# Performance work log

Hardware: AMD Instinct MI355X
Metric: run time of the kernel (lower is better)

Reference implementation:

```python
import jax, jax.numpy as jnp
import numpy as np

N, E, D_IN, HID, OUT, H = 20000, 320000, 128, 128, 128, 4

def _lin(key, fan_in, fan_out):
    kw, kb = jax.random.split(key)
    W = jax.random.normal(kw, (fan_in, fan_out), jnp.float32) * 0.05
    b = jax.random.normal(kb, (fan_out,), jnp.float32) * 0.05
    return W, b

def setup_inputs() -> dict:
    key = jax.random.key(0)
    ks = jax.random.split(key, 10)
    x = jax.random.normal(ks[0], (N, D_IN), jnp.float32)
    edge_index = jax.random.randint(ks[1], (2, E), 0, N, jnp.int32)
    # Layer 0: TransformerConv(D_IN -> HID, heads=H, concat=True)
    Wq0, bq0 = _lin(ks[2], D_IN, H * HID)
    Wk0, bk0 = _lin(ks[3], D_IN, H * HID)
    Wv0, bv0 = _lin(ks[4], D_IN, H * HID)
    Ws0, bs0 = _lin(ks[5], D_IN, H * HID)   # root/skip projection
    # Layer 1: TransformerConv(H*HID -> OUT, heads=H, concat=False)
    Wq1, bq1 = _lin(ks[6], H * HID, H * OUT)
    Wk1, bk1 = _lin(ks[7], H * HID, H * OUT)
    Wv1, bv1 = _lin(ks[8], H * HID, H * OUT)
    Ws1, bs1 = _lin(ks[9], H * HID, OUT)    # skip maps to OUT when concat=False
    return dict(x=x, edge_index=edge_index,
                Wq0=Wq0, bq0=bq0, Wk0=Wk0, bk0=bk0, Wv0=Wv0, bv0=bv0, Ws0=Ws0, bs0=bs0,
                Wq1=Wq1, bq1=bq1, Wk1=Wk1, bk1=bk1, Wv1=Wv1, bv1=bv1, Ws1=Ws1, bs1=bs1)

def _transformer_conv(x, src, dst, Wq, bq, Wk, bk, Wv, bv, Ws, bs, heads, out_ch, concat):
    n = x.shape[0]
    q = (x @ Wq + bq).reshape(n, heads, out_ch)
    k = (x @ Wk + bk).reshape(n, heads, out_ch)
    v = (x @ Wv + bv).reshape(n, heads, out_ch)
    # per-edge attention logits: [E, H]
    alpha = jnp.einsum('ehc,ehc->eh', q[dst], k[src]) / jnp.sqrt(jnp.float32(out_ch))
    # softmax grouped by destination node (numerically stable)
    m = jax.ops.segment_max(alpha, dst, num_segments=n)        # [N, H]
    alpha = jnp.exp(alpha - m[dst])
    s = jax.ops.segment_sum(alpha, dst, num_segments=n)       # [N, H]
    alpha = alpha / (s[dst] + 1e-16)
    # weighted scatter-add of messages: [N, H, C]
    out = jax.ops.segment_sum(alpha[..., None] * v[src], dst, num_segments=n)
    if concat:
        out = out.reshape(n, heads * out_ch)
    else:
        out = out.mean(axis=1)
    return out + x @ Ws + bs  # root weight (skip connection)

def reference(x, edge_index,
              Wq0, bq0, Wk0, bk0, Wv0, bv0, Ws0, bs0,
              Wq1, bq1, Wk1, bk1, Wv1, bv1, Ws1, bs1):
    src, dst = edge_index[0], edge_index[1]
    h = _transformer_conv(x, src, dst, Wq0, bq0, Wk0, bk0, Wv0, bv0, Ws0, bs0, H, HID, True)
    h = jax.nn.relu(h)  # dropout is identity in eval mode
    out = _transformer_conv(h, src, dst, Wq1, bq1, Wk1, bk1, Wv1, bv1, Ws1, bs1, H, OUT, False)
    return out
```

## Files before the change

### kernel.cpp

```cpp
#include <hip/hip_runtime.h>
#include <hip/hip_bf16.h>
#include <math.h>

#define HCH    512
#define OUTD   128
#define N0CAT  2048
#define N1CAT  1664
#define P0STR  1024
#define P1STR  640
#define KVW    1024
#define DCAP   64

typedef __attribute__((ext_vector_type(8))) short short8v;
typedef __attribute__((ext_vector_type(8))) unsigned short ushort8v;
typedef __attribute__((ext_vector_type(4))) unsigned short ushort4v;
typedef __attribute__((ext_vector_type(4))) float floatx4;
typedef __attribute__((ext_vector_type(2))) float floatx2;
typedef __attribute__((ext_vector_type(4))) unsigned int uintx4;

__device__ inline float bf2f(unsigned short u) {
    return __uint_as_float(((unsigned)u) << 16);
}

__device__ inline unsigned short f2bf(float f) {
    return (unsigned short)__bfloat16_as_ushort(__float2bfloat16(f));
}

template <bool HI>
__device__ inline floatx2 fp8x2_to_f32(unsigned int w) {
    return __builtin_amdgcn_cvt_pk_f32_fp8(w, HI);
}

__device__ inline unsigned int f32x4_to_fp8(float a, float b, float c, float d) {
    int w = __builtin_amdgcn_cvt_pk_fp8_f32(a, b, 0, false);
    w = __builtin_amdgcn_cvt_pk_fp8_f32(c, d, w, true);
    return (unsigned int)w;
}

__device__ inline void gload_lds16(const void* g, void* l) {
    __builtin_amdgcn_global_load_lds(
        (const __attribute__((address_space(1))) unsigned int*)g,
        (__attribute__((address_space(3))) unsigned int*)l, 16, 0, 0);
}


__device__ void tpose_tile(const float* __restrict__ W, __hip_bfloat16* __restrict__ o,
                           int K, int C, int bx, int by, int t, float (*tile)[33],
                           int pmode) {
    int c0 = bx * 32, k0 = by * 32;
    int tx = t & 31, ty = t >> 5;
    #pragma unroll
    for (int r = ty; r < 32; r += 8)
        tile[r][tx] = W[(size_t)(k0 + r) * C + c0 + tx];
    __syncthreads();
    #pragma unroll
    for (int r = ty; r < 32; r += 8) {
        int col = c0 + r;
        if (pmode) col = ((col >> 3) << 4) + (col & 7) + ((pmode == 2) ? 8 : 0);
        o[(size_t)col * K + k0 + tx] = __float2bfloat16(tile[tx][r]);
    }
}

__global__ __launch_bounds__(256) void prep_all(
        const float* __restrict__ x, __hip_bfloat16* __restrict__ Xb,
        const float* __restrict__ Wq0, const float* __restrict__ Wk0,
        const float* __restrict__ Wv0, const float* __restrict__ Ws0,
        const float* __restrict__ Wq1, const float* __restrict__ Wk1,
        const float* __restrict__ Wv1, const float* __restrict__ Ws1,
        const float* __restrict__ bq0, const float* __restrict__ bk0,
        const float* __restrict__ bv0, const float* __restrict__ bs0,
        const float* __restrict__ bq1, const float* __restrict__ bk1,
        const float* __restrict__ bv1, const float* __restrict__ bs1,
        __hip_bfloat16* __restrict__ Wc0, __hip_bfloat16* __restrict__ Wc1,
        float* __restrict__ bc0, float* __restrict__ bc1,
        int* __restrict__ deg, int* __restrict__ srcs,
        const int* __restrict__ srce, const int* __restrict__ dste,
        int N, int E) {
    __shared__ float tile[32][33];
    int t = threadIdx.x;
    int b = blockIdx.x;
    int nb_cast = (N * 128 + 255) >> 8;
    if (b < nb_cast) {
        int i = b * 256 + t;
        if (i < N * 128) Xb[i] = __float2bfloat16(x[i]);
        return;
    }
    b -= nb_cast;
    if (b < 256) {
        int z = b >> 6, rem = b & 63;
        const float* W = (z == 0) ? Wq0 : (z == 1) ? Wk0 : (z == 2) ? Wv0 : Ws0;
        int base = (z == 0) ? 0 : (z == 3) ? 1536 : 512;
        int pmode = (z == 1) ? 1 : (z == 2) ? 2 : 0;
        tpose_tile(W, Wc0 + (size_t)base * 128, 128, 512, rem & 15, rem >> 4, t, tile, pmode);
        return;
    }
    b -= 256;
    if (b < 768) {
        int z = b >> 8, rem = b & 255;
        const float* W = (z == 0) ? Wq1 : (z == 1) ? Wk1 : Wv1;
        int base = (z == 0) ? 0 : 512;
        int pmode = (z == 1) ? 1 : (z == 2) ? 2 : 0;
        tpose_tile(W, Wc1 + (size_t)base * 512, 512, 512, rem & 15, rem >> 4, t, tile, pmode);
        return;
    }
    b -= 768;
    if (b < 64) {
        tpose_tile(Ws1, Wc1 + (size_t)1536 * 512, 512, 128, b & 3, b >> 2, t, tile, 0);
        return;
    }
    b -= 64;
    if (b < 8) {
        int i = b * 256 + t;
        if (i < N0CAT) {
            int sel = i >> 9, col = i & 511;
            const float* bb = (sel == 0) ? bq0 : (sel == 1) ? bk0 : (sel == 2) ? bv0 : bs0;
            int d = (sel == 0) ? i
                  : (sel == 3) ? i
                  : 512 + ((col >> 3) << 4) + (col & 7) + ((sel == 2) ? 8 : 0);
            bc0[d] = bb[col];
        }
        if (i < N1CAT) {
            if (i < 1536) {
                int sel = i >> 9, col = i & 511;
                const float* bb = (sel == 0) ? bq1 : (sel == 1) ? bk1 : bv1;
                int d = (sel == 0) ? i
                      : 512 + ((col >> 3) << 4) + (col & 7) + ((sel == 2) ? 8 : 0);
                bc1[d] = bb[col];
            } else {
                bc1[i] = bs1[i - 1536];
            }
        }
        return;
    }
    b -= 8;
    {
        int e = b * 256 + t;
        if (e < E) {
            int d = dste[e];
            int pos = atomicAdd(&deg[d], 1);
            if (pos < DCAP) srcs[d * DCAP + pos] = srce[e];
        }
    }
}


__device__ inline void gemm_store(floatx4 a, const float* __restrict__ bias,
                                  __hip_bfloat16* __restrict__ P, int pstride,
                                  unsigned char* __restrict__ KV8,
                                  int row, int col) {
    floatx4 bv = *(const floatx4*)(bias + col);
    float v0 = a[0] + bv[0];
    float v1 = a[1] + bv[1];
    float v2 = a[2] + bv[2];
    float v3 = a[3] + bv[3];
    if (col < 512) {
        ushort4v o = { f2bf(v0), f2bf(v1), f2bf(v2), f2bf(v3) };
        *(ushort4v*)(P + (size_t)row * pstride + col) = o;
    } else if (col < 1536) {
        *(unsigned int*)(KV8 + (size_t)row * KVW + (col - 512)) = f32x4_to_fp8(v0, v1, v2, v3);
    } else {
        ushort4v o = { f2bf(v0), f2bf(v1), f2bf(v2), f2bf(v3) };
        *(ushort4v*)(P + (size_t)row * pstride + 512 + (col - 1536)) = o;
    }
}


#define BM 128
#define BN 128
#define BK 64

__global__ __launch_bounds__(256) void gemm_mfma(const __hip_bfloat16* __restrict__ A,
                                                 const __hip_bfloat16* __restrict__ Bt,
                                                 const float* __restrict__ bias,
                                                 __hip_bfloat16* __restrict__ P,
                                                 int pstride,
                                                 unsigned char* __restrict__ KV8,
                                                 int M, int K, int Nd, int mt_pad) {
    __shared__ __hip_bfloat16 As[BM][BK];
    __shared__ __hip_bfloat16 Bs[BN][BK];
    int f = blockIdx.x;
    int mt = f % mt_pad, nt = f / mt_pad;
    int bm = mt * BM, bn = nt * BN;
    if (bm >= M) return;
    int t = threadIdx.x;
    int lane = t & 63, w = t >> 6;
    int quad = lane >> 4, l16 = lane & 15;
    int wm = (w >> 1) * 64, wn = (w & 1) * 64;

    int srow = w * 8 + (lane >> 3);
    int c8g = (lane & 7) ^ ((lane >> 3) & 7);
    const char* Ab = (const char*)(A + (size_t)(bm + srow) * K + c8g * 8);
    const char* Bb = (const char*)(Bt + (size_t)(bn + srow) * K + c8g * 8);
    char* Al = (char*)&As[0][0] + w * 1024;
    char* Bl = (char*)&Bs[0][0] + w * 1024;

    int sw = l16 & 7;

    floatx4 acc[4][4];
    #pragma unroll
    for (int i = 0; i < 4; i++)
        #pragma unroll
        for (int j = 0; j < 4; j++)
            acc[i][j] = (floatx4)0.0f;

    for (int k0 = 0; k0 < K; k0 += BK) {
        __syncthreads();
        #pragma unroll
        for (int i = 0; i < 4; i++) {
            size_t go = ((size_t)i * 32 * K + k0) * 2;
            gload_lds16(Ab + go, Al + i * 4096);
            gload_lds16(Bb + go, Bl + i * 4096);
        }
        __syncthreads();
        #pragma unroll
        for (int ks = 0; ks < BK; ks += 32) {
            int c8a = (quad + (ks >> 3)) ^ sw;
            short8v af[4], bfr[4];
            #pragma unroll
            for (int i = 0; i < 4; i++)
                af[i] = *(const short8v*)&As[wm + i * 16 + l16][c8a * 8];
            #pragma unroll
            for (int j = 0; j < 4; j++)
                bfr[j] = *(const short8v*)&Bs[wn + j * 16 + l16][c8a * 8];
            #pragma unroll
            for (int i = 0; i < 4; i++)
                #pragma unroll
                for (int j = 0; j < 4; j++)
                    acc[i][j] = __builtin_amdgcn_mfma_f32_16x16x32_bf16(bfr[j], af[i], acc[i][j], 0, 0, 0);
        }
    }

    #pragma unroll
    for (int i = 0; i < 4; i++) {
        int row = bm + wm + i * 16 + l16;
        if (row >= M) continue;
        #pragma unroll
        for (int j = 0; j < 4; j++)
            gemm_store(acc[i][j], bias, P, pstride, KV8, row, bn + wn + j * 16 + quad * 4);
    }
}


#define L0K 128

__global__ __launch_bounds__(256) void gemm_mfma_l0(const __hip_bfloat16* __restrict__ A,
                                                    const __hip_bfloat16* __restrict__ Bt,
                                                    const float* __restrict__ bias,
                                                    __hip_bfloat16* __restrict__ P,
                                                    int pstride,
                                                    unsigned char* __restrict__ KV8,
                                                    int M, int Nd, int mt_pad) {
    __shared__ __hip_bfloat16 As[128][L0K];
    __shared__ __hip_bfloat16 Bs[128][L0K];
    int f = blockIdx.x;
    int mt = f % mt_pad, nt = f / mt_pad;
    int bm = mt * 128, bn = nt * 128;
    if (bm >= M) return;
    int t = threadIdx.x;
    int lane = t & 63, w = t >> 6;
    int quad = lane >> 4, l16 = lane & 15;
    int wm = (w >> 1) * 64, wn = (w & 1) * 64;

    int srow16 = t >> 4;
    int g = t & 15;
    char* Al = (char*)&As[0][0] + w * 1024;
    char* Bl = (char*)&Bs[0][0] + w * 1024;

    #pragma unroll
    for (int r = 0; r < 8; r++) {
        int row = r * 16 + srow16;
        int sg = g ^ (row & 7);
        gload_lds16((const char*)(A + (size_t)(bm + row) * L0K + sg * 8), Al + r * 4096);
        gload_lds16((const char*)(Bt + (size_t)(bn + row) * L0K + sg * 8), Bl + r * 4096);
    }
    __syncthreads();

    int sw = l16 & 7;
    floatx4 acc[4][4];
    #pragma unroll
    for (int i = 0; i < 4; i++)
        #pragma unroll
        for (int j = 0; j < 4; j++)
            acc[i][j] = (floatx4)0.0f;

    #pragma unroll
    for (int ks = 0; ks < L0K; ks += 32) {
        int c8a = (quad + (ks >> 3)) ^ sw;
        short8v af[4], bfr[4];
        #pragma unroll
        for (int i = 0; i < 4; i++)
            af[i] = *(const short8v*)&As[wm + i * 16 + l16][c8a * 8];
        #pragma unroll
        for (int j = 0; j < 4; j++)
            bfr[j] = *(const short8v*)&Bs[wn + j * 16 + l16][c8a * 8];
        #pragma unroll
        for (int i = 0; i < 4; i++)
            #pragma unroll
            for (int j = 0; j < 4; j++)
                acc[i][j] = __builtin_amdgcn_mfma_f32_16x16x32_bf16(bfr[j], af[i], acc[i][j], 0, 0, 0);
    }

    #pragma unroll
    for (int i = 0; i < 4; i++) {
        int row = bm + wm + i * 16 + l16;
        if (row >= M) continue;
        #pragma unroll
        for (int j = 0; j < 4; j++)
            gemm_store(acc[i][j], bias, P, pstride, KV8, row, bn + wn + j * 16 + quad * 4);
    }
}


#define PF 4

__global__ __launch_bounds__(256) void attn_kernel(const __hip_bfloat16* __restrict__ P,
                                                   int pstride,
                                                   const unsigned char* __restrict__ KV8,
                                                   const int* __restrict__ deg,
                                                   const int* __restrict__ srcs,
                                                   __hip_bfloat16* __restrict__ out_b,
                                                   float* __restrict__ out_f,
                                                   int n_nodes, int mode) {
    int wave = threadIdx.x >> 6;
    int lane = threadIdx.x & 63;
    int node = blockIdx.x * 4 + wave;
    if (node >= n_nodes) return;
    const float qsc = 0.08838834764831845f * 1.4426950408889634f;

    const __hip_bfloat16* Prow = P + (size_t)node * pstride;
    floatx2 q2[4];
    {
        ushort8v qu = *(const ushort8v*)(Prow + lane * 8);
        #pragma unroll
        for (int j = 0; j < 4; j++) {
            q2[j][0] = bf2f(qu[2 * j])     * qsc;
            q2[j][1] = bf2f(qu[2 * j + 1]) * qsc;
        }
    }

    float l = 0.f;
    floatx2 acc2[4];
    #pragma unroll
    for (int j = 0; j < 4; j++) acc2[j] = (floatx2)0.0f;

    int cnt = deg[node];
    if (cnt > DCAP) cnt = DCAP;
    const int* ep = srcs + (size_t)node * DCAP;
    const unsigned char* Kb = KV8 + lane * 16;

    uintx4 kv[PF];
    #pragma unroll
    for (int i = 0; i < PF; i++) {
        if (i < cnt) {
            int s = ep[i];
            kv[i] = *(const uintx4*)(Kb + (size_t)s * KVW);
        }
    }

    int e = 0;
    for (; e + PF <= cnt; e += PF) {
        #pragma unroll
        for (int i = 0; i < PF; i++) {
            uintx4 u = kv[i];
            int pe = e + i + PF;
            if (pe < cnt) {
                int s = ep[pe];
                kv[i] = *(const uintx4*)(Kb + (size_t)s * KVW);
            }
            floatx2 k01 = fp8x2_to_f32<false>(u[0]);
            floatx2 k23 = fp8x2_to_f32<true >(u[0]);
            floatx2 k45 = fp8x2_to_f32<false>(u[1]);
            floatx2 k67 = fp8x2_to_f32<true >(u[1]);
            floatx2 d2 = q2[0] * k01;
            d2 += q2[1] * k23;
            d2 += q2[2] * k45;
            d2 += q2[3] * k67;
            float part = d2[0] + d2[1];
            part += __shfl_xor(part, 1);
            part += __shfl_xor(part, 2);
            part += __shfl_xor(part, 4);
            part += __shfl_xor(part, 8);
            float p = exp2f(part);
            l += p;
            floatx2 pv = { p, p };
            floatx2 v01 = fp8x2_to_f32<false>(u[2]);
            floatx2 v23 = fp8x2_to_f32<true >(u[2]);
            floatx2 v45 = fp8x2_to_f32<false>(u[3]);
            floatx2 v67 = fp8x2_to_f32<true >(u[3]);
            acc2[0] += pv * v01;
            acc2[1] += pv * v23;
            acc2[2] += pv * v45;
            acc2[3] += pv * v67;
        }
    }
    #pragma unroll
    for (int i = 0; i < PF; i++) {
        if (e + i < cnt) {
            uintx4 u = kv[i];
            floatx2 k01 = fp8x2_to_f32<false>(u[0]);
            floatx2 k23 = fp8x2_to_f32<true >(u[0]);
            floatx2 k45 = fp8x2_to_f32<false>(u[1]);
            floatx2 k67 = fp8x2_to_f32<true >(u[1]);
            floatx2 d2 = q2[0] * k01;
            d2 += q2[1] * k23;
            d2 += q2[2] * k45;
            d2 += q2[3] * k67;
            float part = d2[0] + d2[1];
            part += __shfl_xor(part, 1);
            part += __shfl_xor(part, 2);
            part += __shfl_xor(part, 4);
            part += __shfl_xor(part, 8);
            float p = exp2f(part);
            l += p;
            floatx2 pv = { p, p };
            floatx2 v01 = fp8x2_to_f32<false>(u[2]);
            floatx2 v23 = fp8x2_to_f32<true >(u[2]);
            floatx2 v45 = fp8x2_to_f32<false>(u[3]);
            floatx2 v67 = fp8x2_to_f32<true >(u[3]);
            acc2[0] += pv * v01;
            acc2[1] += pv * v23;
            acc2[2] += pv * v45;
            acc2[3] += pv * v67;
        }
    }
    float inv = (l > 0.f) ? 1.f / l : 0.f;

    if (mode == 0) {
        ushort8v su = *(const ushort8v*)(Prow + 512 + lane * 8);
        ushort8v o;
        #pragma unroll
        for (int j = 0; j < 8; j++) {
            float r = fmaxf(acc2[j >> 1][j & 1] * inv + bf2f(su[j]), 0.f);
            o[j] = f2bf(r);
        }
        *(ushort8v*)(out_b + (size_t)node * HCH + lane * 8) = o;
    } else {
        float r[8];
        #pragma unroll
        for (int j = 0; j < 8; j++) {
            r[j] = acc2[j >> 1][j & 1] * inv;
            r[j] += __shfl_xor(r[j], 16);
            r[j] += __shfl_xor(r[j], 32);
            r[j] *= 0.25f;
        }
        if (lane < 16) {
            const __hip_bfloat16* sp = Prow + 512 + lane * 8;
            float* op = out_f + (size_t)node * OUTD + lane * 8;
            #pragma unroll
            for (int j = 0; j < 8; j++) op[j] = r[j] + bf2f(__bfloat16_as_ushort(sp[j]));
        }
    }
}


static inline size_t align256(size_t x) { return (x + 255) & ~(size_t)255; }

extern "C" void kernel_launch(void* const* d_in, const int* in_sizes, int n_in,
                              void* d_out, int out_size, void* d_ws, size_t ws_size,
                              hipStream_t stream) {
    const float* x   = (const float*)d_in[0];
    const int*   ei  = (const int*)d_in[1];
    const float* Wq0 = (const float*)d_in[2];  const float* bq0 = (const float*)d_in[3];
    const float* Wk0 = (const float*)d_in[4];  const float* bk0 = (const float*)d_in[5];
    const float* Wv0 = (const float*)d_in[6];  const float* bv0 = (const float*)d_in[7];
    const float* Ws0 = (const float*)d_in[8];  const float* bs0 = (const float*)d_in[9];
    const float* Wq1 = (const float*)d_in[10]; const float* bq1 = (const float*)d_in[11];
    const float* Wk1 = (const float*)d_in[12]; const float* bk1 = (const float*)d_in[13];
    const float* Wv1 = (const float*)d_in[14]; const float* bv1 = (const float*)d_in[15];
    const float* Ws1 = (const float*)d_in[16]; const float* bs1 = (const float*)d_in[17];
    float* out = (float*)d_out;

    const int N = in_sizes[0] / 128;
    const int E = in_sizes[1] / 2;
    const int* src = ei;
    const int* dst = ei + E;

    int mtiles = (N + BM - 1) / BM;
    int mt_pad = (mtiles + 7) & ~7;
    const int Mpad = mt_pad * BM;

    char* ws = (char*)d_ws;
    __hip_bfloat16* P0  = (__hip_bfloat16*)ws; ws += align256((size_t)N * P0STR * 2);
    __hip_bfloat16* P1  = P0;
    __hip_bfloat16* Hbb = (__hip_bfloat16*)ws; ws += align256((size_t)Mpad * HCH * 2);
    __hip_bfloat16* Xb  = (__hip_bfloat16*)ws; ws += align256((size_t)Mpad * 128 * 2);
    unsigned char* KV8  = (unsigned char*)ws;  ws += align256((size_t)N * KVW);
    __hip_bfloat16* Wc0 = (__hip_bfloat16*)ws; ws += align256((size_t)N0CAT * 128 * 2);
    __hip_bfloat16* Wc1 = (__hip_bfloat16*)ws; ws += align256((size_t)N1CAT * 512 * 2);
    float* bc0 = (float*)ws; ws += align256((size_t)N0CAT * 4);
    float* bc1 = (float*)ws; ws += align256((size_t)N1CAT * 4);
    int* deg    = (int*)ws; ws += align256((size_t)N * 4);
    int* srcs   = (int*)ws; ws += align256((size_t)N * DCAP * 4);

    dim3 blk(256);

    hipMemsetAsync(deg, 0, (size_t)N * 4, stream);

    int nb_cast = (N * 128 + 255) / 256;
    int nb_bucket = (E + 255) / 256;
    int nb_prep = nb_cast + 256 + 768 + 64 + 8 + nb_bucket;
    prep_all<<<nb_prep, blk, 0, stream>>>(
        x, Xb, Wq0, Wk0, Wv0, Ws0, Wq1, Wk1, Wv1, Ws1,
        bq0, bk0, bv0, bs0, bq1, bk1, bv1, bs1,
        Wc0, Wc1, bc0, bc1, deg, srcs, src, dst, N, E);

    gemm_mfma_l0<<<dim3(mt_pad * (N0CAT / 128)), blk, 0, stream>>>(
        Xb, Wc0, bc0, P0, P0STR, KV8, N, N0CAT, mt_pad);
    attn_kernel<<<(N + 3) / 4, blk, 0, stream>>>(P0, P0STR, KV8, deg, srcs, Hbb, nullptr, N, 0);

    gemm_mfma<<<dim3(mt_pad * (N1CAT / BN)), blk, 0, stream>>>(
        Hbb, Wc1, bc1, P1, P1STR, KV8, N, 512, N1CAT, mt_pad);
    attn_kernel<<<(N + 3) / 4, blk, 0, stream>>>(P1, P1STR, KV8, deg, srcs, nullptr, out, N, 1);
}
```

Baseline: 317.8 us.

## Load B fragments directly to registers and double-buffer A tiles in GEMMs

Both GEMM kernels stop staging the B (weight) tile through LDS. Each wave now loads its B MFMA fragments straight from global memory into registers, which removes the B LDS writes and reads. The general GEMM also double-buffers the A tile in LDS and prefetches the next K-step's A and B while computing the current one, with one barrier per step instead of two. In exchange it uses more registers and makes uncoalesced-ish direct global reads of B that rely on cache reuse across waves.

```diff
diff --git a/kernel.cpp b/kernel.cpp
--- a/kernel.cpp
+++ b/kernel.cpp
@@ -176,8 +176,7 @@
                                                  int pstride,
                                                  unsigned char* __restrict__ KV8,
                                                  int M, int K, int Nd, int mt_pad) {
-    __shared__ __hip_bfloat16 As[BM][BK];
-    __shared__ __hip_bfloat16 Bs[BN][BK];
+    __shared__ __hip_bfloat16 As[2][BM][BK];
     int f = blockIdx.x;
     int mt = f % mt_pad, nt = f / mt_pad;
     int bm = mt * BM, bn = nt * BN;
@@ -190,11 +189,13 @@
     int srow = w * 8 + (lane >> 3);
     int c8g = (lane & 7) ^ ((lane >> 3) & 7);
     const char* Ab = (const char*)(A + (size_t)(bm + srow) * K + c8g * 8);
-    const char* Bb = (const char*)(Bt + (size_t)(bn + srow) * K + c8g * 8);
-    char* Al = (char*)&As[0][0] + w * 1024;
-    char* Bl = (char*)&Bs[0][0] + w * 1024;
-
+    char* Al = (char*)&As[0][0][0] + w * 1024;
     int sw = l16 & 7;
+
+    const __hip_bfloat16* Brow[4];
+    #pragma unroll
+    for (int j = 0; j < 4; j++)
+        Brow[j] = Bt + (size_t)(bn + wn + j * 16 + l16) * K + quad * 8;
 
     floatx4 acc[4][4];
     #pragma unroll
@@ -203,30 +204,50 @@
         for (int j = 0; j < 4; j++)
             acc[i][j] = (floatx4)0.0f;
 
-    for (int k0 = 0; k0 < K; k0 += BK) {
-        __syncthreads();
-        #pragma unroll
-        for (int i = 0; i < 4; i++) {
-            size_t go = ((size_t)i * 32 * K + k0) * 2;
-            gload_lds16(Ab + go, Al + i * 4096);
-            gload_lds16(Bb + go, Bl + i * 4096);
-        }
-        __syncthreads();
-        #pragma unroll
-        for (int ks = 0; ks < BK; ks += 32) {
-            int c8a = (quad + (ks >> 3)) ^ sw;
-            short8v af[4], bfr[4];
+    auto stageA = [&](int k0, int b) {
+        #pragma unroll
+        for (int i = 0; i < 4; i++)
+            gload_lds16(Ab + ((size_t)i * 32 * K + k0) * 2, Al + b * (BM * BK * 2) + i * 4096);
+    };
+
+    short8v bg0[2][4], bg1[2][4];
+    auto loadB = [&](int k0, short8v (*bg)[4]) {
+        #pragma unroll
+        for (int ks = 0; ks < 2; ks++)
+            #pragma unroll
+            for (int j = 0; j < 4; j++)
+                bg[ks][j] = *(const short8v*)(Brow[j] + k0 + ks * 32);
+    };
+
+    auto compute = [&](int b, short8v (*bg)[4]) {
+        #pragma unroll
+        for (int ks = 0; ks < 2; ks++) {
+            int c8a = (quad + ks * 4) ^ sw;
+            short8v af[4];
             #pragma unroll
             for (int i = 0; i < 4; i++)
-                af[i] = *(const short8v*)&As[wm + i * 16 + l16][c8a * 8];
-            #pragma unroll
-            for (int j = 0; j < 4; j++)
-                bfr[j] = *(const short8v*)&Bs[wn + j * 16 + l16][c8a * 8];
+                af[i] = *(const short8v*)&As[b][wm + i * 16 + l16][c8a * 8];
             #pragma unroll
             for (int i = 0; i < 4; i++)
                 #pragma unroll
                 for (int j = 0; j < 4; j++)
-                    acc[i][j] = __builtin_amdgcn_mfma_f32_16x16x32_bf16(bfr[j], af[i], acc[i][j], 0, 0, 0);
+                    acc[i][j] = __builtin_amdgcn_mfma_f32_16x16x32_bf16(bg[ks][j], af[i], acc[i][j], 0, 0, 0);
+        }
+    };
+
+    stageA(0, 0);
+    loadB(0, bg0);
+    __syncthreads();
+
+    int nk = K / BK;
+    for (int tt = 0; tt < nk; tt += 2) {
+        if (tt + 1 < nk) { stageA((tt + 1) * BK, 1); loadB((tt + 1) * BK, bg1); }
+        compute(0, bg0);
+        __syncthreads();
+        if (tt + 1 < nk) {
+            if (tt + 2 < nk) { stageA((tt + 2) * BK, 0); loadB((tt + 2) * BK, bg0); }
+            compute(1, bg1);
+            __syncthreads();
         }
     }
 
@@ -251,7 +272,6 @@
                                                     unsigned char* __restrict__ KV8,
                                                     int M, int Nd, int mt_pad) {
     __shared__ __hip_bfloat16 As[128][L0K];
-    __shared__ __hip_bfloat16 Bs[128][L0K];
     int f = blockIdx.x;
     int mt = f % mt_pad, nt = f / mt_pad;
     int bm = mt * 128, bn = nt * 128;
@@ -264,15 +284,25 @@
     int srow16 = t >> 4;
     int g = t & 15;
     char* Al = (char*)&As[0][0] + w * 1024;
-    char* Bl = (char*)&Bs[0][0] + w * 1024;
 
     #pragma unroll
     for (int r = 0; r < 8; r++) {
         int row = r * 16 + srow16;
         int sg = g ^ (row & 7);
         gload_lds16((const char*)(A + (size_t)(bm + row) * L0K + sg * 8), Al + r * 4096);
-        gload_lds16((const char*)(Bt + (size_t)(bn + row) * L0K + sg * 8), Bl + r * 4096);
-    }
+    }
+
+    const __hip_bfloat16* Brow[4];
+    #pragma unroll
+    for (int j = 0; j < 4; j++)
+        Brow[j] = Bt + (size_t)(bn + wn + j * 16 + l16) * L0K + quad * 8;
+    short8v bg[4][4];
+    #pragma unroll
+    for (int ks = 0; ks < 4; ks++)
+        #pragma unroll
+        for (int j = 0; j < 4; j++)
+            bg[ks][j] = *(const short8v*)(Brow[j] + ks * 32);
+
     __syncthreads();
 
     int sw = l16 & 7;
@@ -284,20 +314,17 @@
             acc[i][j] = (floatx4)0.0f;
 
     #pragma unroll
-    for (int ks = 0; ks < L0K; ks += 32) {
-        int c8a = (quad + (ks >> 3)) ^ sw;
-        short8v af[4], bfr[4];
+    for (int ks = 0; ks < 4; ks++) {
+        int c8a = (quad + ks * 4) ^ sw;
+        short8v af[4];
         #pragma unroll
         for (int i = 0; i < 4; i++)
             af[i] = *(const short8v*)&As[wm + i * 16 + l16][c8a * 8];
-        #pragma unroll
-        for (int j = 0; j < 4; j++)
-            bfr[j] = *(const short8v*)&Bs[wn + j * 16 + l16][c8a * 8];
         #pragma unroll
         for (int i = 0; i < 4; i++)
             #pragma unroll
             for (int j = 0; j < 4; j++)
-                acc[i][j] = __builtin_amdgcn_mfma_f32_16x16x32_bf16(bfr[j], af[i], acc[i][j], 0, 0, 0);
+                acc[i][j] = __builtin_amdgcn_mfma_f32_16x16x32_bf16(bg[ks][j], af[i], acc[i][j], 0, 0, 0);
     }
 
     #pragma unroll
```

New measurement: 419.4 us. 1.32x slower.
